# Kernel tuning notes

Measured on AMD Instinct MI355X. Metric: run time of the kernel, lower is better.

## Reference

```python
import jax, jax.numpy as jnp
import numpy as np

GROUPS = 32
EPS = 1e-5


def _group_norm(x, scale, bias):
    B, C, H, W = x.shape
    xg = x.reshape(B, GROUPS, -1)
    mu = xg.mean(axis=-1, keepdims=True)
    var = jnp.mean(jnp.square(xg - mu), axis=-1, keepdims=True)
    xn = ((xg - mu) * jax.lax.rsqrt(var + EPS)).reshape(B, C, H, W)
    return xn * scale[None, :, None, None] + bias[None, :, None, None]


def _conv1x1(x, w, b):
    # x: [B,C,H,W], w: [O,C], b: [O]
    return jnp.einsum('bchw,oc->bohw', x, w) + b[None, :, None, None]


def setup_inputs() -> dict:
    key = jax.random.key(0)
    ks = jax.random.split(key, 6)
    B, C, H, W = 16, 512, 32, 32
    x = jax.random.normal(ks[0], (B, C, H, W), dtype=jnp.float32)
    # xavier_uniform for [C, C, 1, 1] conv: limit = sqrt(6 / (fan_in + fan_out)) = sqrt(6 / (2C))
    lim = float(np.sqrt(6.0 / (2 * C)))
    wq = jax.random.uniform(ks[1], (C, C), jnp.float32, -lim, lim)
    wk = jax.random.uniform(ks[2], (C, C), jnp.float32, -lim, lim)
    wv = jax.random.uniform(ks[3], (C, C), jnp.float32, -lim, lim)
    wo = jax.random.uniform(ks[4], (C, C), jnp.float32, -lim, lim) * 1e-5  # gain=1e-5
    zeros_c = jnp.zeros((C,), jnp.float32)
    return {
        'x': x,
        'gn_scale': jnp.ones((C,), jnp.float32),
        'gn_bias': zeros_c,
        'wq': wq, 'bq': zeros_c,
        'wk': wk, 'bk': zeros_c,
        'wv': wv, 'bv': zeros_c,
        'wo': wo, 'bo': zeros_c,
    }


def reference(x, gn_scale, gn_bias, wq, bq, wk, bk, wv, bv, wo, bo):
    B, C, H, W = x.shape
    N = H * W
    h = _group_norm(x, gn_scale, gn_bias)
    q = _conv1x1(h, wq, bq).reshape(B, C, N)  # [B,C,N]
    k = _conv1x1(h, wk, bk).reshape(B, C, N)
    v = _conv1x1(h, wv, bv).reshape(B, C, N)
    scale = 1.0 / jnp.sqrt(jnp.asarray(C, x.dtype))
    w = jnp.einsum('bcn,bcm->bnm', q, k) * scale  # [B,N,N]
    w = jax.nn.softmax(w, axis=-1)
    hv = jnp.einsum('bnm,bcm->bcn', w, v).reshape(B, C, H, W)
    out = _conv1x1(hv, wo, bo)
    return x + out
```

## Files before the change

kernel.cpp:

```cpp
#include <hip/hip_runtime.h>
#include <hip/hip_bf16.h>
#include <cstdint>

typedef unsigned char u8;
typedef float floatx4 __attribute__((ext_vector_type(4)));
typedef int intx8 __attribute__((ext_vector_type(8)));

__device__ __forceinline__ void gld_lds16(const void* g, void* l) {
    __builtin_amdgcn_global_load_lds(
        (const __attribute__((address_space(1))) unsigned int*)g,
        (__attribute__((address_space(3))) unsigned int*)l, 16, 0, 0);
}

__device__ __forceinline__ u8 f2fp8(float v) {
    return (u8)(__builtin_amdgcn_cvt_pk_fp8_f32(v, v, 0, false) & 0xff);
}
__device__ __forceinline__ unsigned int pack4_fp8(float a, float b, float c, float d) {
    unsigned int u = __builtin_amdgcn_cvt_pk_fp8_f32(a, b, 0, false);
    u = __builtin_amdgcn_cvt_pk_fp8_f32(c, d, u, true);
    return u;
}

__device__ __forceinline__ intx8 ld_frag(const u8* p, int lo, int hi) {
    uint4 a = *(const uint4*)(p + lo);
    uint4 b = *(const uint4*)(p + hi);
    intx8 r;
    r[0] = a.x; r[1] = a.y; r[2] = a.z; r[3] = a.w;
    r[4] = b.x; r[5] = b.y; r[6] = b.z; r[7] = b.w;
    return r;
}
__device__ __forceinline__ intx8 ld_frag_g(const u8* p) {
    uint4 a = *(const uint4*)(p);
    uint4 b = *(const uint4*)(p + 16);
    intx8 r;
    r[0] = a.x; r[1] = a.y; r[2] = a.z; r[3] = a.w;
    r[4] = b.x; r[5] = b.y; r[6] = b.z; r[7] = b.w;
    return r;
}


__global__ __launch_bounds__(256) void setup_kernel(
    const float* __restrict__ x, const float* __restrict__ gs,
    const float* __restrict__ gb,
    const float* __restrict__ wq, const float* __restrict__ wk,
    const float* __restrict__ wv, const float* __restrict__ wo,
    const float* __restrict__ bq, const float* __restrict__ bk,
    const float* __restrict__ bv,
    u8* __restrict__ hT, u8* __restrict__ wqkv, u8* __restrict__ wob,
    float* __restrict__ bqkv, float* __restrict__ lsum)
{
    const int t = threadIdx.x;
    if (blockIdx.x >= 512) {
        int i = (blockIdx.x - 512) * 256 + t;
        if (i < 786432) {
            int which = i >> 18;
            int off = i & 262143;
            const float* src = which == 0 ? wq : which == 1 ? wk : wv;
            wqkv[i] = f2fp8(src[off]);
        } else {
            wob[i - 786432] = f2fp8(wo[i - 786432] * 262144.0f);
        }
        if (i < 1536)
            bqkv[i] = i < 512 ? bq[i] : (i < 1024 ? bk[i - 512] : bv[i - 1024]);
        if (i < 16384)
            lsum[i] = 0.0f;
        return;
    }
    const int b = blockIdx.x >> 5;
    const int g = blockIdx.x & 31;
    const int wave = t >> 6, lane = t & 63;
    const float4* x4 = (const float4*)(x + ((long long)b * 512 + g * 16) * 1024);

    float4 v[16];
    float s1 = 0.f, s2 = 0.f;
#pragma unroll
    for (int i = 0; i < 16; ++i) {
        v[i] = x4[i * 256 + t];
        s1 += v[i].x + v[i].y + v[i].z + v[i].w;
        s2 += v[i].x * v[i].x + v[i].y * v[i].y + v[i].z * v[i].z + v[i].w * v[i].w;
    }
#pragma unroll
    for (int m = 32; m; m >>= 1) {
        s1 += __shfl_xor(s1, m, 64);
        s2 += __shfl_xor(s2, m, 64);
    }
    __shared__ float red[2][4];
    __shared__ float stats[2];
    if (lane == 0) { red[0][wave] = s1; red[1][wave] = s2; }
    __syncthreads();
    if (t == 0) {
        float a = red[0][0] + red[0][1] + red[0][2] + red[0][3];
        float q = red[1][0] + red[1][1] + red[1][2] + red[1][3];
        float mu = a * (1.0f / 16384.0f);
        float var = q * (1.0f / 16384.0f) - mu * mu;
        stats[0] = mu;
        stats[1] = rsqrtf(var + 1e-5f);
    }
    __syncthreads();
    const float mu = stats[0], rs = stats[1];

#pragma unroll
    for (int i = 0; i < 16; ++i) {
        const float sc = gs[g * 16 + i] * rs;
        const float bi = gb[g * 16 + i] - mu * sc;
        v[i].x = v[i].x * sc + bi;
        v[i].y = v[i].y * sc + bi;
        v[i].z = v[i].z * sc + bi;
        v[i].w = v[i].w * sc + bi;
    }
    u8* hb = hT + (long long)b * 524288 + g * 16;
#pragma unroll
    for (int r = 0; r < 4; ++r) {
        uint4 o;
        o.x = pack4_fp8(v[0][r],  v[1][r],  v[2][r],  v[3][r]);
        o.y = pack4_fp8(v[4][r],  v[5][r],  v[6][r],  v[7][r]);
        o.z = pack4_fp8(v[8][r],  v[9][r],  v[10][r], v[11][r]);
        o.w = pack4_fp8(v[12][r], v[13][r], v[14][r], v[15][r]);
        *(uint4*)(hb + (long long)(4 * t + r) * 512) = o;
    }
}

template <int EPI>
__global__ __launch_bounds__(256, 3) void gemm_mx(
    const u8* __restrict__ A, long long sA,
    const u8* __restrict__ B, long long sB,
    void* __restrict__ C, long long sC,
    void* __restrict__ C2, void* __restrict__ C3,
    int ldC, int K,
    const float* __restrict__ bias,
    const float* __restrict__ resid, long long sR,
    float scale, float* __restrict__ lsum)
{
    __shared__ __align__(16) u8 smem[33792];
    const int tid = threadIdx.x;
    const int l = tid & 63;
    const int wave = tid >> 6;
    const int wm = wave >> 1, wn = wave & 1;
    const int bm = blockIdx.x, bn = blockIdx.y, b = blockIdx.z;

    const u8* Ab = A + (long long)b * sA + (long long)bm * 128 * K;
    const u8* Bb = B + (long long)b * sB + (long long)bn * 128 * K;

    const int srow = wave * 8 + (l >> 3);
    const int sg = ((l & 7) ^ ((l >> 3) & 7)) * 16;
    const u8* ga  = Ab + (long long)srow * K + sg;
    const u8* gbp = Bb + (long long)srow * K + sg;
    const long long c32 = (long long)32 * K;
    const int ldst = wave * 1024;

    const int q4 = l >> 4;
    const int glo = ((2 * q4) ^ (l & 7)) * 16;
    const int ghi = ((2 * q4 + 1) ^ (l & 7)) * 16;
    int arow[4], brow[4];
#pragma unroll
    for (int i = 0; i < 4; ++i) {
        arow[i] = (wm * 64 + i * 16 + (l & 15)) * 128;
        brow[i] = (wn * 64 + i * 16 + (l & 15)) * 128 + 16384;
    }

    floatx4 acc[4][4] = {};
    const int niter = K >> 7;

    for (int it = 0; it < niter; ++it) {
        const int k0 = it << 7;
#pragma unroll
        for (int c = 0; c < 4; ++c) {
            gld_lds16(ga + c * c32 + k0, smem + c * 4096 + ldst);
            gld_lds16(gbp + c * c32 + k0, smem + 16384 + c * 4096 + ldst);
        }
        __syncthreads();
        intx8 bfr[4];
#pragma unroll
        for (int j = 0; j < 4; ++j) bfr[j] = ld_frag(smem + brow[j], glo, ghi);
#pragma unroll
        for (int i = 0; i < 4; ++i) {
            intx8 af = ld_frag(smem + arow[i], glo, ghi);
#pragma unroll
            for (int j = 0; j < 4; ++j)
                acc[i][j] = __builtin_amdgcn_mfma_scale_f32_16x16x128_f8f6f4(
                    af, bfr[j], acc[i][j], 0, 0, 0, 127, 0, 127);
        }
        __syncthreads();
    }

    if (EPI == 3) {
        float* Cf = (float*)C;
#pragma unroll
        for (int i = 0; i < 4; ++i) {
            const int mrow = bm * 128 + wm * 64 + i * 16 + q4 * 4;
#pragma unroll
            for (int j = 0; j < 4; ++j) {
                const int ncol = bn * 128 + wn * 64 + j * 16 + (l & 15);
#pragma unroll
                for (int r = 0; r < 4; ++r) {
                    const int row = mrow + r;
                    float v = acc[i][j][r] * scale + bias[row] +
                              resid[(long long)b * sR + (long long)row * ldC + ncol];
                    Cf[(long long)b * sC + (long long)row * ldC + ncol] = v;
                }
            }
        }
    } else if (EPI == 1) {
        const int which = bn >> 2;
        u8* tile = smem;
#pragma unroll
        for (int i = 0; i < 4; ++i) {
            const int rl = wm * 64 + i * 16 + q4 * 4;
#pragma unroll
            for (int j = 0; j < 4; ++j) {
                const int cl = wn * 64 + j * 16 + (l & 15);
                const float badd = bias[bn * 128 + cl];
                if (which == 2) {
                    *(unsigned int*)(tile + cl * 144 + rl) =
                        pack4_fp8(acc[i][j][0] + badd, acc[i][j][1] + badd,
                                  acc[i][j][2] + badd, acc[i][j][3] + badd);
                } else {
#pragma unroll
                    for (int r = 0; r < 4; ++r)
                        tile[(rl + r) * 144 + cl] = f2fp8(acc[i][j][r] + badd);
                }
            }
        }
        __syncthreads();
        const int w2  = wave >> 1;
        const int cbl = (wave & 1) * 2 + (l >> 5);
        const int lnw = (l >> 1) & 15;
        const int g16 = (l & 1) * 16;
#pragma unroll
        for (int p = 0; p < 4; ++p) {
            const int rtile = p * 2 + w2;
            uint4 dd = *(const uint4*)(tile + (rtile * 16 + lnw) * 144 + cbl * 32 + g16);
            u8* dst;
            if (which == 0)
                dst = (u8*)C + (long long)b * sC + (long long)(bm * 8 + rtile) * 8192
                      + ((bn & 3) * 4 + cbl) * 512 + lnw * 32 + g16;
            else if (which == 1)
                dst = (u8*)C2 + (long long)b * sC + (long long)(bm * 8 + rtile) * 8192
                      + ((bn & 3) * 4 + cbl) * 512 + lnw * 32 + g16;
            else
                dst = (u8*)C3 + (long long)b * sC + (long long)((bn & 3) * 8 + rtile) * 16384
                      + (long long)(bm * 4 + cbl) * 512 + lnw * 32 + g16;
            *(uint4*)dst = dd;
        }
    }
}

__global__ __launch_bounds__(256, 2) void attn_core(
    const u8* __restrict__ qg, const u8* __restrict__ kg,
    const u8* __restrict__ vg, u8* __restrict__ hvT)
{
    __shared__ __align__(16) u8 smem[8704];
    const int tid = threadIdx.x;
    const int l = tid & 63;
    const int w = tid >> 6;
    const int d = blockIdx.x;
    const int b  = (d & 7) * 2 + ((d >> 8) & 1);
    const int bq = (d >> 3) & 31;

    const u8* qb = qg + (long long)b * 524288 + (long long)(bq * 2) * 8192;
    const u8* kb = kg + (long long)b * 524288;
    const u8* vb = vg + (long long)b * 524288;

    const int q4 = l >> 4;
    const int ln = l & 15;
    const int glo = ((2 * q4) ^ (l & 7)) * 16;
    const int ghi = ((2 * q4 + 1) ^ (l & 7)) * 16;
    const int lo32 = ln * 32;

    intx8 qf[2][4];
#pragma unroll
    for (int j = 0; j < 2; ++j)
#pragma unroll
        for (int kc = 0; kc < 4; ++kc)
            qf[j][kc] = ld_frag_g(qb + j * 8192 + (kc * 4 + q4) * 512 + lo32);

    floatx4 acc_pv[8][2] = {};
    float psum[2] = {0.f, 0.f};
    const float scale = 0.044194173824159216f;

    for (int mt = 0; mt < 8; ++mt) {
        u8* E = smem + (mt & 1) * 4096;
        floatx4 acc_s[2][2] = {};
#pragma unroll
        for (int kc = 0; kc < 4; ++kc) {
#pragma unroll
            for (int i = 0; i < 2; ++i) {
                intx8 kf = ld_frag_g(kb + (long long)(mt * 8 + w * 2 + i) * 8192
                                        + (kc * 4 + q4) * 512 + lo32);
#pragma unroll
                for (int j = 0; j < 2; ++j)
                    acc_s[i][j] = __builtin_amdgcn_mfma_scale_f32_16x16x128_f8f6f4(
                        kf, qf[j][kc], acc_s[i][j], 0, 0, 0, 127, 0, 127);
            }
        }
        intx8 vfA[4], vfB[4];
        const u8* vrow = vb + (long long)(w * 8) * 16384 + (mt * 4 + q4) * 512 + lo32;
#pragma unroll
        for (int i = 0; i < 4; ++i)
            vfA[i] = ld_frag_g(vrow + (long long)i * 16384);
#pragma unroll
        for (int i = 0; i < 2; ++i) {
#pragma unroll
            for (int j = 0; j < 2; ++j) {
                float e0 = __expf(acc_s[i][j][0] * scale);
                float e1 = __expf(acc_s[i][j][1] * scale);
                float e2 = __expf(acc_s[i][j][2] * scale);
                float e3 = __expf(acc_s[i][j][3] * scale);
                psum[j] += e0 + e1 + e2 + e3;
                const int n = j * 16 + ln;
                const int m0 = w * 32 + i * 16 + q4 * 4;
                *(unsigned int*)(E + n * 128 + (m0 ^ ((n & 7) * 16))) =
                    pack4_fp8(e0 * 0.25f, e1 * 0.25f, e2 * 0.25f, e3 * 0.25f);
            }
        }
        __syncthreads();
#pragma unroll
        for (int i = 0; i < 4; ++i)
            vfB[i] = ld_frag_g(vrow + (long long)(i + 4) * 16384);
        intx8 ef[2];
#pragma unroll
        for (int j = 0; j < 2; ++j)
            ef[j] = ld_frag(E + (j * 16 + ln) * 128, glo, ghi);
#pragma unroll
        for (int i = 0; i < 4; ++i)
#pragma unroll
            for (int j = 0; j < 2; ++j)
                acc_pv[i][j] = __builtin_amdgcn_mfma_scale_f32_16x16x128_f8f6f4(
                    vfA[i], ef[j], acc_pv[i][j], 0, 0, 0, 127, 0, 127);
#pragma unroll
        for (int i = 0; i < 4; ++i)
#pragma unroll
            for (int j = 0; j < 2; ++j)
                acc_pv[i + 4][j] = __builtin_amdgcn_mfma_scale_f32_16x16x128_f8f6f4(
                    vfB[i], ef[j], acc_pv[i + 4][j], 0, 0, 0, 127, 0, 127);
    }

#pragma unroll
    for (int j = 0; j < 2; ++j) {
        psum[j] += __shfl_xor(psum[j], 16, 64);
        psum[j] += __shfl_xor(psum[j], 32, 64);
    }
    float* sb = (float*)(smem + 8192);
    if (l < 16) {
        sb[w * 32 + l]      = psum[0];
        sb[w * 32 + 16 + l] = psum[1];
    }
    __syncthreads();
    float rln[2];
#pragma unroll
    for (int j = 0; j < 2; ++j) {
        const int n = j * 16 + ln;
        rln[j] = 4.0f / (sb[n] + sb[32 + n] + sb[64 + n] + sb[96 + n]);
    }
    u8* ob = hvT + (long long)b * 524288 + (long long)(bq * 32) * 512;
#pragma unroll
    for (int i = 0; i < 8; ++i) {
#pragma unroll
        for (int j = 0; j < 2; ++j) {
            const int n = j * 16 + ln;
            const int c = w * 128 + i * 16 + q4 * 4;
            *(unsigned int*)(ob + (long long)n * 512 + c) =
                pack4_fp8(acc_pv[i][j][0] * rln[j], acc_pv[i][j][1] * rln[j],
                          acc_pv[i][j][2] * rln[j], acc_pv[i][j][3] * rln[j]);
        }
    }
}

extern "C" void kernel_launch(void* const* d_in, const int* in_sizes, int n_in,
                              void* d_out, int out_size, void* d_ws, size_t ws_size,
                              hipStream_t stream)
{
    const float* x  = (const float*)d_in[0];
    const float* gs = (const float*)d_in[1];
    const float* gb = (const float*)d_in[2];
    const float* wq = (const float*)d_in[3];
    const float* bq = (const float*)d_in[4];
    const float* wk = (const float*)d_in[5];
    const float* bk = (const float*)d_in[6];
    const float* wv = (const float*)d_in[7];
    const float* bv = (const float*)d_in[8];
    const float* wo = (const float*)d_in[9];
    const float* bo = (const float*)d_in[10];
    float* out = (float*)d_out;

    u8* p = (u8*)d_ws;
    u8* hT   = p; p += 8388608;
    u8* q    = p; p += 8388608;
    u8* k    = p; p += 8388608;
    u8* v    = p; p += 8388608;
    u8* wqkv = p; p += 786432;
    float* bqkv = (float*)p; p += 6144;
    u8* wob  = p; p += 262144;
    u8* P    = p; p += 16777216;
    u8* hvT  = p; p += 8388608;
    float* lsum = (float*)p; p += 65536;
    (void)P;

    setup_kernel<<<4608, 256, 0, stream>>>(x, gs, gb, wq, wk, wv, wo, bq, bk, bv,
                                           hT, wqkv, wob, bqkv, lsum);

    gemm_mx<1><<<dim3(8, 12, 16), 256, 0, stream>>>(
        hT, 524288LL, wqkv, 0LL, q, 524288LL, k, v,
        512, 512, bqkv, nullptr, 0LL, 1.0f, nullptr);

    attn_core<<<dim3(512, 1, 1), 256, 0, stream>>>(q, k, v, hvT);

    gemm_mx<3><<<dim3(4, 8, 16), 256, 0, stream>>>(
        wob, 0LL, hvT, 524288LL, out, 524288LL, nullptr, nullptr,
        1024, 512, bo, x, 524288LL, 3.814697265625e-06f, nullptr);
}
```

Before: 175.2 us.

## Pre-tile GEMM operands into fragment-major layout and load MFMA fragments directly from global

The producers (setup kernel for hT and weights, attn_core for hvT) now write operands in a 16-row x 32-byte blocked layout that matches the MFMA fragment order. The GEMM drops its LDS staging loop with global_load_lds and barriers, and each wave reads its fragments straight from global memory with K fixed at compile time and the loop fully unrolled. This removes LDS traffic and syncthreads. In exchange, operand reuse across waves now depends on the caches, and the shared buffer is kept only for the epilogue. The unused lsum and P workspace buffers are also removed.

```diff
diff --git a/kernel.cpp b/kernel.cpp
--- a/kernel.cpp
+++ b/kernel.cpp
@@ -5,12 +5,6 @@
 typedef unsigned char u8;
 typedef float floatx4 __attribute__((ext_vector_type(4)));
 typedef int intx8 __attribute__((ext_vector_type(8)));
-
-__device__ __forceinline__ void gld_lds16(const void* g, void* l) {
-    __builtin_amdgcn_global_load_lds(
-        (const __attribute__((address_space(1))) unsigned int*)g,
-        (__attribute__((address_space(3))) unsigned int*)l, 16, 0, 0);
-}
 
 __device__ __forceinline__ u8 f2fp8(float v) {
     return (u8)(__builtin_amdgcn_cvt_pk_fp8_f32(v, v, 0, false) & 0xff);
@@ -47,7 +41,7 @@
     const float* __restrict__ bq, const float* __restrict__ bk,
     const float* __restrict__ bv,
     u8* __restrict__ hT, u8* __restrict__ wqkv, u8* __restrict__ wob,
-    float* __restrict__ bqkv, float* __restrict__ lsum)
+    float* __restrict__ bqkv)
 {
     const int t = threadIdx.x;
     if (blockIdx.x >= 512) {
@@ -56,14 +50,17 @@
             int which = i >> 18;
             int off = i & 262143;
             const float* src = which == 0 ? wq : which == 1 ? wk : wv;
-            wqkv[i] = f2fp8(src[off]);
+            int row = i >> 9, col = i & 511;
+            wqkv[(long long)(row >> 4) * 8192 + (col >> 5) * 512
+                 + (row & 15) * 32 + (col & 31)] = f2fp8(src[off]);
         } else {
-            wob[i - 786432] = f2fp8(wo[i - 786432] * 262144.0f);
+            int i2 = i - 786432;
+            int row = i2 >> 9, col = i2 & 511;
+            wob[(long long)(row >> 4) * 8192 + (col >> 5) * 512
+                + (row & 15) * 32 + (col & 31)] = f2fp8(wo[i2] * 262144.0f);
         }
         if (i < 1536)
             bqkv[i] = i < 512 ? bq[i] : (i < 1024 ? bk[i - 512] : bv[i - 1024]);
-        if (i < 16384)
-            lsum[i] = 0.0f;
         return;
     }
     const int b = blockIdx.x >> 5;
@@ -108,79 +105,61 @@
         v[i].z = v[i].z * sc + bi;
         v[i].w = v[i].w * sc + bi;
     }
-    u8* hb = hT + (long long)b * 524288 + g * 16;
+    u8* hb = hT + (long long)b * 524288 + (g >> 1) * 512 + (g & 1) * 16;
 #pragma unroll
     for (int r = 0; r < 4; ++r) {
+        const int pos = 4 * t + r;
         uint4 o;
         o.x = pack4_fp8(v[0][r],  v[1][r],  v[2][r],  v[3][r]);
         o.y = pack4_fp8(v[4][r],  v[5][r],  v[6][r],  v[7][r]);
         o.z = pack4_fp8(v[8][r],  v[9][r],  v[10][r], v[11][r]);
         o.w = pack4_fp8(v[12][r], v[13][r], v[14][r], v[15][r]);
-        *(uint4*)(hb + (long long)(4 * t + r) * 512) = o;
-    }
-}
-
-template <int EPI>
+        *(uint4*)(hb + (long long)(pos >> 4) * 8192 + (pos & 15) * 32) = o;
+    }
+}
+
+template <int EPI, int K>
 __global__ __launch_bounds__(256, 3) void gemm_mx(
     const u8* __restrict__ A, long long sA,
     const u8* __restrict__ B, long long sB,
     void* __restrict__ C, long long sC,
     void* __restrict__ C2, void* __restrict__ C3,
-    int ldC, int K,
+    int ldC,
     const float* __restrict__ bias,
     const float* __restrict__ resid, long long sR,
-    float scale, float* __restrict__ lsum)
+    float scale)
 {
-    __shared__ __align__(16) u8 smem[33792];
+    __shared__ __align__(16) u8 smem[18432];
     const int tid = threadIdx.x;
     const int l = tid & 63;
     const int wave = tid >> 6;
     const int wm = wave >> 1, wn = wave & 1;
     const int bm = blockIdx.x, bn = blockIdx.y, b = blockIdx.z;
 
-    const u8* Ab = A + (long long)b * sA + (long long)bm * 128 * K;
-    const u8* Bb = B + (long long)b * sB + (long long)bn * 128 * K;
-
-    const int srow = wave * 8 + (l >> 3);
-    const int sg = ((l & 7) ^ ((l >> 3) & 7)) * 16;
-    const u8* ga  = Ab + (long long)srow * K + sg;
-    const u8* gbp = Bb + (long long)srow * K + sg;
-    const long long c32 = (long long)32 * K;
-    const int ldst = wave * 1024;
-
     const int q4 = l >> 4;
-    const int glo = ((2 * q4) ^ (l & 7)) * 16;
-    const int ghi = ((2 * q4 + 1) ^ (l & 7)) * 16;
-    int arow[4], brow[4];
-#pragma unroll
-    for (int i = 0; i < 4; ++i) {
-        arow[i] = (wm * 64 + i * 16 + (l & 15)) * 128;
-        brow[i] = (wn * 64 + i * 16 + (l & 15)) * 128 + 16384;
-    }
+    const int ln = l & 15;
+    const long long rbs = (long long)16 * K;
+
+    const u8* Ab = A + (long long)b * sA + (long long)bm * 128 * K
+                   + (long long)(wm * 4) * rbs + q4 * 512 + ln * 32;
+    const u8* Bb = B + (long long)b * sB + (long long)bn * 128 * K
+                   + (long long)(wn * 4) * rbs + q4 * 512 + ln * 32;
 
     floatx4 acc[4][4] = {};
-    const int niter = K >> 7;
-
-    for (int it = 0; it < niter; ++it) {
-        const int k0 = it << 7;
-#pragma unroll
-        for (int c = 0; c < 4; ++c) {
-            gld_lds16(ga + c * c32 + k0, smem + c * 4096 + ldst);
-            gld_lds16(gbp + c * c32 + k0, smem + 16384 + c * 4096 + ldst);
-        }
-        __syncthreads();
-        intx8 bfr[4];
-#pragma unroll
-        for (int j = 0; j < 4; ++j) bfr[j] = ld_frag(smem + brow[j], glo, ghi);
+#pragma unroll
+    for (int kc = 0; kc < (K >> 7); ++kc) {
+        intx8 bf[4];
+#pragma unroll
+        for (int j = 0; j < 4; ++j)
+            bf[j] = ld_frag_g(Bb + (long long)j * rbs + kc * 2048);
 #pragma unroll
         for (int i = 0; i < 4; ++i) {
-            intx8 af = ld_frag(smem + arow[i], glo, ghi);
+            intx8 af = ld_frag_g(Ab + (long long)i * rbs + kc * 2048);
 #pragma unroll
             for (int j = 0; j < 4; ++j)
                 acc[i][j] = __builtin_amdgcn_mfma_scale_f32_16x16x128_f8f6f4(
-                    af, bfr[j], acc[i][j], 0, 0, 0, 127, 0, 127);
-        }
-        __syncthreads();
+                    af, bf[j], acc[i][j], 0, 0, 0, 127, 0, 127);
+        }
     }
 
     if (EPI == 3) {
@@ -190,7 +169,7 @@
             const int mrow = bm * 128 + wm * 64 + i * 16 + q4 * 4;
 #pragma unroll
             for (int j = 0; j < 4; ++j) {
-                const int ncol = bn * 128 + wn * 64 + j * 16 + (l & 15);
+                const int ncol = bn * 128 + wn * 64 + j * 16 + ln;
 #pragma unroll
                 for (int r = 0; r < 4; ++r) {
                     const int row = mrow + r;
@@ -208,7 +187,7 @@
             const int rl = wm * 64 + i * 16 + q4 * 4;
 #pragma unroll
             for (int j = 0; j < 4; ++j) {
-                const int cl = wn * 64 + j * 16 + (l & 15);
+                const int cl = wn * 64 + j * 16 + ln;
                 const float badd = bias[bn * 128 + cl];
                 if (which == 2) {
                     *(unsigned int*)(tile + cl * 144 + rl) =
@@ -352,14 +331,13 @@
         const int n = j * 16 + ln;
         rln[j] = 4.0f / (sb[n] + sb[32 + n] + sb[64 + n] + sb[96 + n]);
     }
-    u8* ob = hvT + (long long)b * 524288 + (long long)(bq * 32) * 512;
+    u8* ob = hvT + (long long)b * 524288 + (long long)(bq * 2) * 8192;
 #pragma unroll
     for (int i = 0; i < 8; ++i) {
 #pragma unroll
         for (int j = 0; j < 2; ++j) {
-            const int n = j * 16 + ln;
             const int c = w * 128 + i * 16 + q4 * 4;
-            *(unsigned int*)(ob + (long long)n * 512 + c) =
+            *(unsigned int*)(ob + j * 8192 + (c >> 5) * 512 + ln * 32 + (c & 31)) =
                 pack4_fp8(acc_pv[i][j][0] * rln[j], acc_pv[i][j][1] * rln[j],
                           acc_pv[i][j][2] * rln[j], acc_pv[i][j][3] * rln[j]);
         }
@@ -391,21 +369,18 @@
     u8* wqkv = p; p += 786432;
     float* bqkv = (float*)p; p += 6144;
     u8* wob  = p; p += 262144;
-    u8* P    = p; p += 16777216;
     u8* hvT  = p; p += 8388608;
-    float* lsum = (float*)p; p += 65536;
-    (void)P;
 
     setup_kernel<<<4608, 256, 0, stream>>>(x, gs, gb, wq, wk, wv, wo, bq, bk, bv,
-                                           hT, wqkv, wob, bqkv, lsum);
-
-    gemm_mx<1><<<dim3(8, 12, 16), 256, 0, stream>>>(
+                                           hT, wqkv, wob, bqkv);
+
+    gemm_mx<1, 512><<<dim3(8, 12, 16), 256, 0, stream>>>(
         hT, 524288LL, wqkv, 0LL, q, 524288LL, k, v,
-        512, 512, bqkv, nullptr, 0LL, 1.0f, nullptr);
+        512, bqkv, nullptr, 0LL, 1.0f);
 
     attn_core<<<dim3(512, 1, 1), 256, 0, stream>>>(q, k, v, hvT);
 
-    gemm_mx<3><<<dim3(4, 8, 16), 256, 0, stream>>>(
+    gemm_mx<3, 512><<<dim3(4, 8, 16), 256, 0, stream>>>(
         wob, 0LL, hvT, 524288LL, out, 524288LL, nullptr, nullptr,
-        1024, 512, bo, x, 524288LL, 3.814697265625e-06f, nullptr);
-}
+        1024, bo, x, 524288LL, 3.814697265625e-06f);
+}
```

Result: slower. 216.9 us (+23.8%).

## Stage output-projection epilogue through LDS for coalesced float4 residual stores

Applied to the files above, without the earlier changes.

The final GEMM epilogue now writes scaled accumulators plus bias into shared memory in two 64-row halves, then reads them back row-major so each thread does coalesced float4 residual loads and output stores. The old version did scattered scalar loads and stores. The change also raises the launch-bounds occupancy hint from 3 to 4 blocks per CU and removes the unused lsum buffer, its zero-fill and the P workspace. The trade-off is extra LDS traffic and barriers, plus register pressure from the tighter occupancy bound.

```diff
diff --git a/kernel.cpp b/kernel.cpp
--- a/kernel.cpp
+++ b/kernel.cpp
@@ -47,7 +47,7 @@
     const float* __restrict__ bq, const float* __restrict__ bk,
     const float* __restrict__ bv,
     u8* __restrict__ hT, u8* __restrict__ wqkv, u8* __restrict__ wob,
-    float* __restrict__ bqkv, float* __restrict__ lsum)
+    float* __restrict__ bqkv)
 {
     const int t = threadIdx.x;
     if (blockIdx.x >= 512) {
@@ -62,8 +62,6 @@
         }
         if (i < 1536)
             bqkv[i] = i < 512 ? bq[i] : (i < 1024 ? bk[i - 512] : bv[i - 1024]);
-        if (i < 16384)
-            lsum[i] = 0.0f;
         return;
     }
     const int b = blockIdx.x >> 5;
@@ -121,7 +119,7 @@
 }
 
 template <int EPI>
-__global__ __launch_bounds__(256, 3) void gemm_mx(
+__global__ __launch_bounds__(256, 4) void gemm_mx(
     const u8* __restrict__ A, long long sA,
     const u8* __restrict__ B, long long sB,
     void* __restrict__ C, long long sC,
@@ -129,7 +127,7 @@
     int ldC, int K,
     const float* __restrict__ bias,
     const float* __restrict__ resid, long long sR,
-    float scale, float* __restrict__ lsum)
+    float scale)
 {
     __shared__ __align__(16) u8 smem[33792];
     const int tid = threadIdx.x;
@@ -149,13 +147,14 @@
     const int ldst = wave * 1024;
 
     const int q4 = l >> 4;
+    const int ln = l & 15;
     const int glo = ((2 * q4) ^ (l & 7)) * 16;
     const int ghi = ((2 * q4 + 1) ^ (l & 7)) * 16;
     int arow[4], brow[4];
 #pragma unroll
     for (int i = 0; i < 4; ++i) {
-        arow[i] = (wm * 64 + i * 16 + (l & 15)) * 128;
-        brow[i] = (wn * 64 + i * 16 + (l & 15)) * 128 + 16384;
+        arow[i] = (wm * 64 + i * 16 + ln) * 128;
+        brow[i] = (wn * 64 + i * 16 + ln) * 128 + 16384;
     }
 
     floatx4 acc[4][4] = {};
@@ -185,20 +184,38 @@
 
     if (EPI == 3) {
         float* Cf = (float*)C;
-#pragma unroll
-        for (int i = 0; i < 4; ++i) {
-            const int mrow = bm * 128 + wm * 64 + i * 16 + q4 * 4;
-#pragma unroll
-            for (int j = 0; j < 4; ++j) {
-                const int ncol = bn * 128 + wn * 64 + j * 16 + (l & 15);
-#pragma unroll
-                for (int r = 0; r < 4; ++r) {
-                    const int row = mrow + r;
-                    float v = acc[i][j][r] * scale + bias[row] +
-                              resid[(long long)b * sR + (long long)row * ldC + ncol];
-                    Cf[(long long)b * sC + (long long)row * ldC + ncol] = v;
+        float* lf = (float*)smem;
+#pragma unroll
+        for (int h = 0; h < 2; ++h) {
+            if (wm == h) {
+#pragma unroll
+                for (int i = 0; i < 4; ++i) {
+#pragma unroll
+                    for (int j = 0; j < 4; ++j) {
+                        const int cl = wn * 64 + j * 16 + ln;
+#pragma unroll
+                        for (int r = 0; r < 4; ++r) {
+                            const int rl = i * 16 + q4 * 4 + r;
+                            lf[rl * 132 + cl] = acc[i][j][r] * scale
+                                + bias[bm * 128 + h * 64 + rl];
+                        }
+                    }
                 }
             }
+            __syncthreads();
+#pragma unroll
+            for (int it = 0; it < 8; ++it) {
+                const int rl = it * 8 + (tid >> 5);
+                const int c4 = (tid & 31) * 4;
+                const long long gro = (long long)b * sR
+                    + (long long)(bm * 128 + h * 64 + rl) * ldC + bn * 128 + c4;
+                float4 vv = *(const float4*)(lf + rl * 132 + c4);
+                const float4 rr = *(const float4*)(resid + gro);
+                vv.x += rr.x; vv.y += rr.y; vv.z += rr.z; vv.w += rr.w;
+                *(float4*)(Cf + (long long)b * sC
+                    + (long long)(bm * 128 + h * 64 + rl) * ldC + bn * 128 + c4) = vv;
+            }
+            __syncthreads();
         }
     } else if (EPI == 1) {
         const int which = bn >> 2;
@@ -208,7 +225,7 @@
             const int rl = wm * 64 + i * 16 + q4 * 4;
 #pragma unroll
             for (int j = 0; j < 4; ++j) {
-                const int cl = wn * 64 + j * 16 + (l & 15);
+                const int cl = wn * 64 + j * 16 + ln;
                 const float badd = bias[bn * 128 + cl];
                 if (which == 2) {
                     *(unsigned int*)(tile + cl * 144 + rl) =
@@ -391,21 +408,18 @@
     u8* wqkv = p; p += 786432;
     float* bqkv = (float*)p; p += 6144;
     u8* wob  = p; p += 262144;
-    u8* P    = p; p += 16777216;
     u8* hvT  = p; p += 8388608;
-    float* lsum = (float*)p; p += 65536;
-    (void)P;
 
     setup_kernel<<<4608, 256, 0, stream>>>(x, gs, gb, wq, wk, wv, wo, bq, bk, bv,
-                                           hT, wqkv, wob, bqkv, lsum);
+                                           hT, wqkv, wob, bqkv);
 
     gemm_mx<1><<<dim3(8, 12, 16), 256, 0, stream>>>(
         hT, 524288LL, wqkv, 0LL, q, 524288LL, k, v,
-        512, 512, bqkv, nullptr, 0LL, 1.0f, nullptr);
+        512, 512, bqkv, nullptr, 0LL, 1.0f);
 
     attn_core<<<dim3(512, 1, 1), 256, 0, stream>>>(q, k, v, hvT);
 
     gemm_mx<3><<<dim3(4, 8, 16), 256, 0, stream>>>(
         wob, 0LL, hvT, 524288LL, out, 524288LL, nullptr, nullptr,
-        1024, 512, bo, x, 524288LL, 3.814697265625e-06f, nullptr);
-}
+        1024, 512, bo, x, 524288LL, 3.814697265625e-06f);
+}
```

Measured after the change: 194.9 us. +11.2%, slower.
